# Performance work log

Hardware: AMD Instinct MI355X
Metric: run time of the kernel (lower is better)

## Reference

```python
import jax, jax.numpy as jnp
import numpy as np
import math
from jax import lax

EPS = 1e-5  # BatchNorm1d default eps
K = 7       # causal conv kernel size
H = 5       # number of heads in block 2


def _cconv(x, w, b):
    # CausalConv1d: left-pad by (K-1)*dilation = 6, then valid conv. x: [B,C,L], w: [O,I,K]
    y = lax.conv_general_dilated(x, w, window_strides=(1,), padding=[(K - 1, 0)],
                                 dimension_numbers=('NCH', 'OIH', 'NCH'))
    return y + b[None, :, None]


def _bn(x, g, b):
    # BatchNorm1d in training mode: batch stats over (N, L) per channel, biased variance
    m = x.mean((0, 2), keepdims=True)
    v = ((x - m) ** 2).mean((0, 2), keepdims=True)
    return g[None, :, None] * (x - m) * lax.rsqrt(v + EPS) + b[None, :, None]


def _attn(x1, x2, x3, scale):
    # sigmoid(((X1 @ X2^T) / sqrt(L)) @ X3); x*: [B,C,L]
    s = jnp.einsum('bcl,bdl->bcd', x1, x2) * scale
    return jax.nn.sigmoid(jnp.einsum('bcd,bdl->bcl', s, x3))


def _attn_heads(x1, x2, x3, scale):
    # 5 heads chunked along L (contiguous chunks) -> vectorized over head axis
    B, C, L = x1.shape
    r = lambda x: x.reshape(B, C, H, L // H)
    x1r, x2r, x3r = r(x1), r(x2), r(x3)
    s = jnp.einsum('bchk,bdhk->bhcd', x1r, x2r) * scale  # scale uses full L, as in source
    a = jax.nn.sigmoid(jnp.einsum('bhcd,bdhk->bchk', s, x3r))
    return a.reshape(B, C, L)


def setup_inputs() -> dict:
    key = jax.random.key(0)
    ks = jax.random.split(key, 20)
    B, C, L = 64, 30, 200
    CL = C * L
    cs = (C * K) ** -0.5   # conv weight scale
    ls = CL ** -0.5        # linear weight scale
    d = {}
    d['X'] = jax.random.normal(ks[0], (B, C, L), jnp.float32)
    for i, nm in enumerate(['b1c1', 'b1c2', 'b1c3', 'b2c1', 'b2c2', 'b2c3']):
        d[nm + '_w'] = jax.random.normal(ks[1 + i], (C, C, K), jnp.float32) * cs
        d[nm + '_b'] = jax.random.normal(ks[7 + i], (C,), jnp.float32) * cs
    for nm in ['bn11', 'bn12', 'bn21', 'bn22']:
        d[nm + '_g'] = jnp.ones((C,), jnp.float32)
        d[nm + '_b'] = jnp.zeros((C,), jnp.float32)
    d['lin1_w'] = jax.random.normal(ks[13], (CL, CL), jnp.float32) * ls
    d['lin1_b'] = jax.random.normal(ks[14], (CL,), jnp.float32) * ls
    d['lin2_w'] = jax.random.normal(ks[15], (CL, CL), jnp.float32) * ls
    d['lin2_b'] = jax.random.normal(ks[16], (CL,), jnp.float32) * ls
    d['cw'] = jax.random.normal(ks[17], (CL, 2 * CL), jnp.float32) * (2 * CL) ** -0.5
    d['cb'] = jax.random.normal(ks[18], (CL,), jnp.float32) * (2 * CL) ** -0.5
    return d


def reference(X, b1c1_w, b1c1_b, b1c2_w, b1c2_b, b1c3_w, b1c3_b,
              bn11_g, bn11_b, lin1_w, lin1_b, lin2_w, lin2_b, bn12_g, bn12_b,
              b2c1_w, b2c1_b, b2c2_w, b2c2_b, b2c3_w, b2c3_b,
              bn21_g, bn21_b, bn22_g, bn22_b, cw, cb):
    B, C, L = X.shape
    scale = 1.0 / math.sqrt(L)
    # block 1: single-head sigmoid attention
    a1 = _attn(_cconv(X, b1c1_w, b1c1_b), _cconv(X, b1c2_w, b1c2_b),
               _cconv(X, b1c3_w, b1c3_b), scale)
    a1 = _bn(a1 + X, bn11_g, bn11_b)
    a1f = a1.reshape(B, -1)
    o1 = (a1f @ lin1_w.T + lin1_b) @ lin2_w.T + lin2_b  # dropout is eval-mode identity
    out1 = _bn(a1 + o1.reshape(B, C, L), bn12_g, bn12_b)
    # block 2: 5-head sigmoid attention
    a2 = _attn_heads(_cconv(X, b2c1_w, b2c1_b), _cconv(X, b2c2_w, b2c2_b),
                     _cconv(X, b2c3_w, b2c3_b), scale)
    a2 = _bn(a2 + X, bn21_g, bn21_b)
    a2f = a2.reshape(B, -1)
    # NOTE: source reuses b1_linearchain for block 2 (b2_linearchain is unused)
    o2 = (a2f @ lin1_w.T + lin1_b) @ lin2_w.T + lin2_b
    out2 = _bn(a2 + o2.reshape(B, C, L), bn22_g, bn22_b)
    # converge
    out = jnp.concatenate([out1, out2], axis=1).reshape(B, -1)  # [B, 2*C*L]
    out = out @ cw.T + cb                                       # [B, C*L]
    return out.reshape(B, 30, -1)
```

## Files before the change

### kernel.cpp

```cpp
#include <hip/hip_runtime.h>
#include <hip/hip_bf16.h>
#include <math.h>

typedef __attribute__((ext_vector_type(4))) float f32x4;
typedef __attribute__((ext_vector_type(8))) __bf16 bf16x8;
typedef __attribute__((ext_vector_type(8))) unsigned short u16x8;

__device__ __forceinline__ unsigned short f2bfu(float f) {
    unsigned u = __builtin_bit_cast(unsigned, f);
    u += 0x7fffu + ((u >> 16) & 1u);
    return (unsigned short)(u >> 16);
}

__device__ __forceinline__ bf16x8 to_bf8(f32x4 x, f32x4 y) {
    bf16x8 o;
#pragma unroll
    for (int j = 0; j < 4; ++j) { o[j] = (__bf16)x[j]; o[j + 4] = (__bf16)y[j]; }
    return o;
}

__device__ __forceinline__ void gload_lds16(const void* g, void* l) {
    __builtin_amdgcn_global_load_lds(
        (__attribute__((address_space(1))) const void*)g,
        (__attribute__((address_space(3))) void*)l, 16, 0, 0);
}

template <int N>
__device__ __forceinline__ void waitcnt_vm() {
    if constexpr (N == 6)      asm volatile("s_waitcnt vmcnt(6)" ::: "memory");
    else if constexpr (N == 5) asm volatile("s_waitcnt vmcnt(5)" ::: "memory");
    else                       asm volatile("s_waitcnt vmcnt(0)" ::: "memory");
}

struct ConvArgs {
    const float* w[6];
    const float* b[6];
};

__global__ __launch_bounds__(256) void conv_all(const float* __restrict__ X,
                                                ConvArgs args,
                                                float* __restrict__ out) {
    __shared__ float Xsp[30][208];
    __shared__ float Wg[30][212];
    const int b = blockIdx.x, j = blockIdx.y;
    const int tid = threadIdx.x;
    const float* xb = X + (size_t)b * 6000;
    for (int i = tid; i < 30 * 208; i += 256) {
        const int ci = i / 208, p = i - ci * 208;
        float v = 0.f;
        if (p >= 6 && p < 206) v = xb[ci * 200 + (p - 6)];
        Xsp[ci][p] = v;
    }
    const float* wsrc = args.w[j];
    for (int i = tid; i < 6300; i += 256) Wg[i / 210][i % 210] = wsrc[i];
    __syncthreads();
    if (tid < 240) {
        const int c = tid >> 3;
        const int strip = tid & 7;
        const int l0 = strip * 25;
        float acc[25];
        const float bias = args.b[j][c];
#pragma unroll
        for (int o = 0; o < 25; ++o) acc[o] = bias;
        for (int ci = 0; ci < 30; ++ci) {
            float wv[7];
#pragma unroll
            for (int kk = 0; kk < 7; ++kk) wv[kk] = Wg[c][ci * 7 + kk];
            float xw[31];
#pragma unroll
            for (int i = 0; i < 31; ++i) xw[i] = Xsp[ci][l0 + i];
#pragma unroll
            for (int o = 0; o < 25; ++o) {
                float a = acc[o];
#pragma unroll
                for (int kk = 0; kk < 7; ++kk) a += xw[o + kk] * wv[kk];
                acc[o] = a;
            }
        }
        float* op = out + ((size_t)j * 64 + b) * 6000 + c * 200 + l0;
#pragma unroll
        for (int o = 0; o < 25; ++o) op[o] = acc[o];
    }
}

__global__ __launch_bounds__(256) void attn_k(const float* __restrict__ conv,
                                              const float* __restrict__ X,
                                              float* __restrict__ A_lin) {
    __shared__ float x1s[30][204], x2s[30][204], x3s[30][204];
    __shared__ float S[5][30][30];
    const int b = blockIdx.x, blk = blockIdx.y;
    const int tid = threadIdx.x;
    const f32x4* c1 = (const f32x4*)(conv + (((size_t)blk * 3 + 0) * 64 + b) * 6000);
    const f32x4* c2 = (const f32x4*)(conv + (((size_t)blk * 3 + 1) * 64 + b) * 6000);
    const f32x4* c3 = (const f32x4*)(conv + (((size_t)blk * 3 + 2) * 64 + b) * 6000);
    for (int i = tid; i < 1500; i += 256) {
        const int c = i / 50, q = i - c * 50;
        *(f32x4*)&x1s[c][q * 4] = c1[i];
        *(f32x4*)&x2s[c][q * 4] = c2[i];
        *(f32x4*)&x3s[c][q * 4] = c3[i];
    }
    __syncthreads();
    const float scale = 7.0710678118654752e-2f;
    if (blk == 0) {
        for (int idx = tid; idx < 900; idx += 256) {
            const int c = idx / 30, d = idx - c * 30;
            f32x4 a4 = {};
            for (int q = 0; q < 50; ++q) {
                const f32x4 x = *(const f32x4*)&x1s[c][q * 4];
                const f32x4 y = *(const f32x4*)&x2s[d][q * 4];
                a4 += x * y;
            }
            S[0][c][d] = (a4[0] + a4[1] + a4[2] + a4[3]) * scale;
        }
    } else {
        for (int idx = tid; idx < 4500; idx += 256) {
            const int h = idx / 900, rem = idx - h * 900;
            const int c = rem / 30, d = rem - c * 30;
            f32x4 a4 = {};
            for (int q = 0; q < 10; ++q) {
                const f32x4 x = *(const f32x4*)&x1s[c][h * 40 + q * 4];
                const f32x4 y = *(const f32x4*)&x2s[d][h * 40 + q * 4];
                a4 += x * y;
            }
            S[h][c][d] = (a4[0] + a4[1] + a4[2] + a4[3]) * scale;
        }
    }
    __syncthreads();
    const float* Xb = X + (size_t)b * 6000;
    float* Ab = A_lin + ((size_t)blk * 64 + b) * 6000;
    for (int u = tid; u < 1500; u += 256) {
        const int c = u / 50, q = u - c * 50;
        const int hh = (blk == 0) ? 0 : (q / 10);
        f32x4 a4 = {};
        for (int d = 0; d < 30; ++d) {
            const float sv = S[hh][c][d];
            const f32x4 v = *(const f32x4*)&x3s[d][q * 4];
            a4 += sv * v;
        }
        const f32x4 xv = *(const f32x4*)(Xb + c * 200 + q * 4);
        f32x4 o;
#pragma unroll
        for (int jj = 0; jj < 4; ++jj)
            o[jj] = 1.f / (1.f + __expf(-a4[jj])) + xv[jj];
        *(f32x4*)(Ab + c * 200 + q * 4) = o;
    }
}

template <bool ADD>
__global__ __launch_bounds__(256) void bn_stats(const float* __restrict__ A,
                                                const float* __restrict__ O,
                                                float* __restrict__ part) {
    const int c = blockIdx.x, h = blockIdx.y, bs = blockIdx.z;
    const int tid = threadIdx.x;
    float s = 0.f, ss = 0.f;
    for (int i = tid; i < 1600; i += 256) {
        const int b = bs * 8 + i / 200, l = i % 200;
        const size_t idx = ((size_t)h * 64 + b) * 6000 + c * 200 + l;
        float v = A[idx];
        if constexpr (ADD) v += O[idx];
        s += v; ss += v * v;
    }
    for (int off = 32; off > 0; off >>= 1) { s += __shfl_down(s, off); ss += __shfl_down(ss, off); }
    __shared__ float rs[4], rss[4];
    const int wave = tid >> 6, lane = tid & 63;
    if (lane == 0) { rs[wave] = s; rss[wave] = ss; }
    __syncthreads();
    if (tid == 0) {
        float* p = part + (((size_t)h * 30 + c) * 8 + bs) * 2;
        p[0] = rs[0] + rs[1] + rs[2] + rs[3];
        p[1] = rss[0] + rss[1] + rss[2] + rss[3];
    }
}

__global__ __launch_bounds__(256) void bn_apply1(float* __restrict__ A,
                                                 unsigned short* __restrict__ Ab,
                                                 const float* __restrict__ part,
                                                 const float* __restrict__ g11,
                                                 const float* __restrict__ b11,
                                                 const float* __restrict__ g21,
                                                 const float* __restrict__ b21) {
    const int c = blockIdx.x, h = blockIdx.y, bs = blockIdx.z;
    const int tid = threadIdx.x;
    const float* p = part + (((size_t)h * 30 + c) * 8) * 2;
    float S = 0.f, SS = 0.f;
#pragma unroll
    for (int k = 0; k < 8; ++k) { S += p[k * 2]; SS += p[k * 2 + 1]; }
    const float mean = S * (1.f / 12800.f);
    const float var = SS * (1.f / 12800.f) - mean * mean;
    const float* gp = h ? g21 : g11;
    const float* bp = h ? b21 : b11;
    const float scale = gp[c] * rsqrtf(var + 1e-5f);
    const float shift = bp[c] - mean * scale;
    for (int i = tid; i < 1600; i += 256) {
        const int b = bs * 8 + i / 200, l = i % 200;
        const size_t idx = ((size_t)h * 64 + b) * 6000 + c * 200 + l;
        const float o = A[idx] * scale + shift;
        A[idx] = o;
        Ab[((size_t)h * 64 + b) * 6016 + c * 200 + l] = f2bfu(o);
    }
    if (c == 0) {
        for (int i = tid; i < 8 * 16; i += 256) {
            const int b = bs * 8 + (i >> 4);
            Ab[((size_t)h * 64 + b) * 6016 + 6000 + (i & 15)] = 0;
        }
    }
}

__global__ __launch_bounds__(256) void bn_apply2(const float* __restrict__ A,
                                                 const float* __restrict__ O,
                                                 unsigned short* __restrict__ Cat,
                                                 const float* __restrict__ part,
                                                 const float* __restrict__ g12,
                                                 const float* __restrict__ b12,
                                                 const float* __restrict__ g22,
                                                 const float* __restrict__ b22) {
    const int c = blockIdx.x, h = blockIdx.y, bs = blockIdx.z;
    const int tid = threadIdx.x;
    const float* p = part + (((size_t)h * 30 + c) * 8) * 2;
    float S = 0.f, SS = 0.f;
#pragma unroll
    for (int k = 0; k < 8; ++k) { S += p[k * 2]; SS += p[k * 2 + 1]; }
    const float mean = S * (1.f / 12800.f);
    const float var = SS * (1.f / 12800.f) - mean * mean;
    const float* gp = h ? g22 : g12;
    const float* bp = h ? b22 : b12;
    const float scale = gp[c] * rsqrtf(var + 1e-5f);
    const float shift = bp[c] - mean * scale;
    for (int i = tid; i < 1600; i += 256) {
        const int b = bs * 8 + i / 200, l = i % 200;
        const size_t idx = ((size_t)h * 64 + b) * 6000 + c * 200 + l;
        const float o = (A[idx] + O[idx]) * scale + shift;
        Cat[(size_t)b * 12000 + (size_t)h * 6000 + c * 200 + l] = f2bfu(o);
    }
}

template <int MT>
__global__ __launch_bounds__(256) void gemm_pipe(const unsigned short* __restrict__ A,
                                                 const float* __restrict__ W,
                                                 unsigned short* __restrict__ P,
                                                 int N, int K, int KA,
                                                 int iters_total, int iters_per) {
    constexpr int M = MT * 16;
    constexpr int WB = 128 * 32 * 4;
    constexpr int AB = M * 32 * 2;
    constexpr int ACH = AB / 1024;
    constexpr int BUFSZ = WB + AB;
    constexpr int VMPS = 4 + ACH / 4;
    __shared__ __align__(16) char lds[2][BUFSZ];

    const int tid = threadIdx.x;
    const int wave = tid >> 6;
    const int lane = tid & 63;
    const int r = lane & 15;
    const int g = lane >> 4;
    const int n0 = blockIdx.x * 128;
    const int s = blockIdx.y;
    const int it0 = s * iters_per;
    int it1 = it0 + iters_per;
    if (it1 > iters_total) it1 = iters_total;
    const int nst = it1 - it0;

    f32x4 acc[MT][2] = {};

    const float* wbase[4];
    const float* wclamp[4];
    int kth[4];
#pragma unroll
    for (int u = 0; u < 4; ++u) {
        const int c = wave + 4 * u;
        const int slot = c * 64 + lane;
        const int row = slot >> 3, jj = slot & 7;
        const int j = jj ^ (row & 7);
        int rn = n0 + row;
        if (rn > N - 1) rn = N - 1;
        wbase[u] = W + (size_t)rn * K + j * 4;
        wclamp[u] = W + (size_t)rn * K + (K - 4);
        kth[u] = K - 4 - j * 4;
    }
    const unsigned short* abase[ACH / 4];
#pragma unroll
    for (int u = 0; u < ACH / 4; ++u) {
        const int c = wave + 4 * u;
        const int slot = c * 64 + lane;
        const int m = slot >> 2, jj = slot & 3;
        const int j = jj ^ ((m >> 1) & 3);
        abase[u] = A + (size_t)m * KA + j * 8;
    }

    auto stage = [&](char* base, int it) {
        const int k0 = it * 32;
#pragma unroll
        for (int u = 0; u < 4; ++u) {
            const float* src = (k0 <= kth[u]) ? (wbase[u] + k0) : wclamp[u];
            gload_lds16(src, base + (wave + 4 * u) * 1024);
        }
        char* ab = base + WB;
#pragma unroll
        for (int u = 0; u < ACH / 4; ++u) {
            gload_lds16(abase[u] + k0, ab + (wave + 4 * u) * 1024);
        }
    };

    auto compute = [&](const char* base) {
        const float* Wb = (const float*)base;
        const unsigned short* Ab = (const unsigned short*)(base + WB);
        bf16x8 bfrag[2];
#pragma unroll
        for (int nt = 0; nt < 2; ++nt) {
            const int wr = (wave + 4 * nt) * 16 + r;
            const f32x4* Wrow = (const f32x4*)(Wb + wr * 32);
            bfrag[nt] = to_bf8(Wrow[(2 * g) ^ (r & 7)], Wrow[(2 * g + 1) ^ (r & 7)]);
        }
#pragma unroll
        for (int mt = 0; mt < MT; ++mt) {
            const int m = mt * 16 + r;
            const bf16x8 afrag = __builtin_bit_cast(
                bf16x8, ((const u16x8*)(Ab + (size_t)m * 32))[g ^ ((m >> 1) & 3)]);
            acc[mt][0] = __builtin_amdgcn_mfma_f32_16x16x32_bf16(afrag, bfrag[0], acc[mt][0], 0, 0, 0);
            acc[mt][1] = __builtin_amdgcn_mfma_f32_16x16x32_bf16(afrag, bfrag[1], acc[mt][1], 0, 0, 0);
        }
    };

    if (nst > 0) {
        stage(&lds[0][0], it0);
        if (nst > 1) {
            stage(&lds[1][0], it0 + 1);
            waitcnt_vm<VMPS>();
        } else {
            waitcnt_vm<0>();
        }
        __builtin_amdgcn_s_barrier();
        __builtin_amdgcn_sched_barrier(0);

        int cur = 0;
        for (int it = it0; it < it1; ++it) {
            compute(&lds[cur][0]);
            __builtin_amdgcn_sched_barrier(0);
            __builtin_amdgcn_s_barrier();
            if (it + 2 < it1) stage(&lds[cur][0], it + 2);
            if (it + 1 < it1) {
                if (it + 2 < it1) waitcnt_vm<VMPS>();
                else              waitcnt_vm<0>();
                __builtin_amdgcn_s_barrier();
                __builtin_amdgcn_sched_barrier(0);
            }
            cur ^= 1;
        }
    }

    unsigned short* Pp = P + (size_t)s * M * N;
#pragma unroll
    for (int nt = 0; nt < 2; ++nt) {
        const int col = n0 + (wave + 4 * nt) * 16 + r;
        if (col < N) {
#pragma unroll
            for (int mt = 0; mt < MT; ++mt) {
#pragma unroll
                for (int rr = 0; rr < 4; ++rr) {
                    const int row = mt * 16 + g * 4 + rr;
                    Pp[(size_t)row * N + col] = f2bfu(acc[mt][nt][rr]);
                }
            }
        }
    }
}

template <bool OUT_BF16>
__global__ __launch_bounds__(256) void reduce_bias(const unsigned short* __restrict__ P,
                                                   const float* __restrict__ bias,
                                                   int KS, int MN, int N, int KOUT,
                                                   float* __restrict__ of,
                                                   unsigned short* __restrict__ ob) {
    const int gid0 = blockIdx.x * 256 + threadIdx.x;
    const int gstr = gridDim.x * 256;
    for (int idx = gid0; idx < MN; idx += gstr) {
        float v = bias[idx % N];
        for (int s = 0; s < KS; ++s) {
            const unsigned u = P[(size_t)s * MN + idx];
            v += __builtin_bit_cast(float, u << 16);
        }
        if constexpr (OUT_BF16) ob[(size_t)(idx / N) * KOUT + (idx % N)] = f2bfu(v);
        else of[idx] = v;
    }
    if constexpr (OUT_BF16) {
        if (KOUT > N) {
            const int M = MN / N, PADW = KOUT - N;
            for (int i = gid0; i < M * PADW; i += gstr)
                ob[(size_t)(i / PADW) * KOUT + N + (i % PADW)] = 0;
        }
    }
}

extern "C" void kernel_launch(void* const* d_in, const int* in_sizes, int n_in,
                              void* d_out, int out_size, void* d_ws, size_t ws_size,
                              hipStream_t stream) {
    (void)in_sizes; (void)n_in; (void)out_size;
    const float* X = (const float*)d_in[0];
    ConvArgs ca;
    for (int j = 0; j < 6; ++j) {
        ca.w[j] = (const float*)d_in[1 + 2 * j];
        ca.b[j] = (const float*)d_in[2 + 2 * j];
    }
    const float* bn11_g = (const float*)d_in[13];
    const float* bn11_b = (const float*)d_in[14];
    const float* bn12_g = (const float*)d_in[15];
    const float* bn12_b = (const float*)d_in[16];
    const float* bn21_g = (const float*)d_in[17];
    const float* bn21_b = (const float*)d_in[18];
    const float* bn22_g = (const float*)d_in[19];
    const float* bn22_b = (const float*)d_in[20];
    const float* lin1_w = (const float*)d_in[21];
    const float* lin1_b = (const float*)d_in[22];
    const float* lin2_w = (const float*)d_in[23];
    const float* lin2_b = (const float*)d_in[24];
    const float* cw = (const float*)d_in[25];
    const float* cb = (const float*)d_in[26];
    float* out = (float*)d_out;

    char* w = (char*)d_ws;
    float* A_lin = (float*)w;
    unsigned short* A_bf = (unsigned short*)(w + 3072000);
    char* U = w + 4612096;
    float* convout = (float*)U;
    unsigned short* T_bf = (unsigned short*)U;
    float* O = (float*)(U + 1540096);
    unsigned short* Cat = (unsigned short*)(U + 4612096);
    float* BNS = (float*)(w + 13828096);
    unsigned short* P = (unsigned short*)(w + 13832192);

    const size_t avail = ws_size > 13832192 ? ws_size - 13832192 : 0;
    int KS12 = (int)(avail / 1536000);
    if (KS12 > 16) KS12 = 16;
    if (KS12 < 1) KS12 = 1;
    int KS3 = (int)(avail / 768000);
    if (KS3 > 20) KS3 = 20;
    if (KS3 < 1) KS3 = 1;

    conv_all<<<dim3(64, 6), 256, 0, stream>>>(X, ca, convout);
    attn_k<<<dim3(64, 2), 256, 0, stream>>>(convout, X, A_lin);
    bn_stats<false><<<dim3(30, 2, 8), 256, 0, stream>>>(A_lin, nullptr, BNS);
    bn_apply1<<<dim3(30, 2, 8), 256, 0, stream>>>(A_lin, A_bf, BNS, bn11_g, bn11_b, bn21_g, bn21_b);

    {
        const int it_tot = 188;
        const int it_per = (it_tot + KS12 - 1) / KS12;
        gemm_pipe<8><<<dim3(47, KS12), 256, 0, stream>>>(A_bf, lin1_w, P, 6000, 6000, 6016, it_tot, it_per);
        reduce_bias<true><<<dim3(768), 256, 0, stream>>>(P, lin1_b, KS12, 768000, 6000, 6016, nullptr, T_bf);
        gemm_pipe<8><<<dim3(47, KS12), 256, 0, stream>>>(T_bf, lin2_w, P, 6000, 6000, 6016, it_tot, it_per);
        reduce_bias<false><<<dim3(768), 256, 0, stream>>>(P, lin2_b, KS12, 768000, 6000, 6000, O, nullptr);
    }

    bn_stats<true><<<dim3(30, 2, 8), 256, 0, stream>>>(A_lin, O, BNS);
    bn_apply2<<<dim3(30, 2, 8), 256, 0, stream>>>(A_lin, O, Cat, BNS, bn12_g, bn12_b, bn22_g, bn22_b);

    {
        const int it_tot = 375;
        const int it_per = (it_tot + KS3 - 1) / KS3;
        gemm_pipe<4><<<dim3(47, KS3), 256, 0, stream>>>(Cat, cw, P, 6000, 12000, 12000, it_tot, it_per);
        reduce_bias<false><<<dim3(768), 256, 0, stream>>>(P, cb, KS3, 384000, 6000, 6000, out, nullptr);
    }
}
```

Measured before the change: 262.0 us.

## Triple-buffer GEMM pipeline, fuse BN stats into apply, lower split-K

The GEMM LDS pipeline grows from double to triple buffering, with prefetch depth 3 and vmcnt waits that depend on how many newer stages are in flight. The separate BN statistics kernels are removed: each apply block now recomputes the full per-channel statistics redundantly, which saves two launches at the cost of about eight times more reads. The split-K factors are capped at 10 instead of 16 and 20, which cuts partial-sum traffic for the reduce kernels but lowers parallelism. The larger LDS footprint may reduce occupancy.

```diff
diff --git a/kernel.cpp b/kernel.cpp
--- a/kernel.cpp
+++ b/kernel.cpp
@@ -25,11 +25,17 @@
         (__attribute__((address_space(3))) void*)l, 16, 0, 0);
 }
 
-template <int N>
-__device__ __forceinline__ void waitcnt_vm() {
-    if constexpr (N == 6)      asm volatile("s_waitcnt vmcnt(6)" ::: "memory");
-    else if constexpr (N == 5) asm volatile("s_waitcnt vmcnt(5)" ::: "memory");
-    else                       asm volatile("s_waitcnt vmcnt(0)" ::: "memory");
+template <int VMPS>
+__device__ __forceinline__ void wait_newer(int newer) {
+    if (newer >= 2) {
+        if constexpr (VMPS == 6) asm volatile("s_waitcnt vmcnt(12)" ::: "memory");
+        else                     asm volatile("s_waitcnt vmcnt(10)" ::: "memory");
+    } else if (newer == 1) {
+        if constexpr (VMPS == 6) asm volatile("s_waitcnt vmcnt(6)" ::: "memory");
+        else                     asm volatile("s_waitcnt vmcnt(5)" ::: "memory");
+    } else {
+        asm volatile("s_waitcnt vmcnt(0)" ::: "memory");
+    }
 }
 
 struct ConvArgs {
@@ -146,51 +152,40 @@
     }
 }
 
-template <bool ADD>
-__global__ __launch_bounds__(256) void bn_stats(const float* __restrict__ A,
-                                                const float* __restrict__ O,
-                                                float* __restrict__ part) {
-    const int c = blockIdx.x, h = blockIdx.y, bs = blockIdx.z;
-    const int tid = threadIdx.x;
-    float s = 0.f, ss = 0.f;
-    for (int i = tid; i < 1600; i += 256) {
-        const int b = bs * 8 + i / 200, l = i % 200;
-        const size_t idx = ((size_t)h * 64 + b) * 6000 + c * 200 + l;
-        float v = A[idx];
-        if constexpr (ADD) v += O[idx];
-        s += v; ss += v * v;
-    }
-    for (int off = 32; off > 0; off >>= 1) { s += __shfl_down(s, off); ss += __shfl_down(ss, off); }
-    __shared__ float rs[4], rss[4];
-    const int wave = tid >> 6, lane = tid & 63;
-    if (lane == 0) { rs[wave] = s; rss[wave] = ss; }
-    __syncthreads();
-    if (tid == 0) {
-        float* p = part + (((size_t)h * 30 + c) * 8 + bs) * 2;
-        p[0] = rs[0] + rs[1] + rs[2] + rs[3];
-        p[1] = rss[0] + rss[1] + rss[2] + rss[3];
-    }
-}
-
-__global__ __launch_bounds__(256) void bn_apply1(float* __restrict__ A,
+__global__ __launch_bounds__(256) void bn_fused1(float* __restrict__ A,
                                                  unsigned short* __restrict__ Ab,
-                                                 const float* __restrict__ part,
                                                  const float* __restrict__ g11,
                                                  const float* __restrict__ b11,
                                                  const float* __restrict__ g21,
                                                  const float* __restrict__ b21) {
     const int c = blockIdx.x, h = blockIdx.y, bs = blockIdx.z;
     const int tid = threadIdx.x;
-    const float* p = part + (((size_t)h * 30 + c) * 8) * 2;
-    float S = 0.f, SS = 0.f;
-#pragma unroll
-    for (int k = 0; k < 8; ++k) { S += p[k * 2]; SS += p[k * 2 + 1]; }
-    const float mean = S * (1.f / 12800.f);
-    const float var = SS * (1.f / 12800.f) - mean * mean;
-    const float* gp = h ? g21 : g11;
-    const float* bp = h ? b21 : b11;
-    const float scale = gp[c] * rsqrtf(var + 1e-5f);
-    const float shift = bp[c] - mean * scale;
+    const size_t cbase = (size_t)h * 64 * 6000 + c * 200;
+    float s = 0.f, ss = 0.f;
+    for (int i = tid; i < 12800; i += 256) {
+        const int b = i / 200, l = i - b * 200;
+        const float v = A[cbase + (size_t)b * 6000 + l];
+        s += v; ss += v * v;
+    }
+    for (int off = 32; off > 0; off >>= 1) { s += __shfl_down(s, off); ss += __shfl_down(ss, off); }
+    __shared__ float rs[4], rss[4];
+    __shared__ float sc_sh, sh_sh;
+    const int wave = tid >> 6, lane = tid & 63;
+    if (lane == 0) { rs[wave] = s; rss[wave] = ss; }
+    __syncthreads();
+    if (tid == 0) {
+        const float S = rs[0] + rs[1] + rs[2] + rs[3];
+        const float SS = rss[0] + rss[1] + rss[2] + rss[3];
+        const float mean = S * (1.f / 12800.f);
+        const float var = SS * (1.f / 12800.f) - mean * mean;
+        const float* gp = h ? g21 : g11;
+        const float* bp = h ? b21 : b11;
+        const float scale = gp[c] * rsqrtf(var + 1e-5f);
+        sc_sh = scale;
+        sh_sh = bp[c] - mean * scale;
+    }
+    __syncthreads();
+    const float scale = sc_sh, shift = sh_sh;
     for (int i = tid; i < 1600; i += 256) {
         const int b = bs * 8 + i / 200, l = i % 200;
         const size_t idx = ((size_t)h * 64 + b) * 6000 + c * 200 + l;
@@ -206,26 +201,42 @@
     }
 }
 
-__global__ __launch_bounds__(256) void bn_apply2(const float* __restrict__ A,
+__global__ __launch_bounds__(256) void bn_fused2(const float* __restrict__ A,
                                                  const float* __restrict__ O,
                                                  unsigned short* __restrict__ Cat,
-                                                 const float* __restrict__ part,
                                                  const float* __restrict__ g12,
                                                  const float* __restrict__ b12,
                                                  const float* __restrict__ g22,
                                                  const float* __restrict__ b22) {
     const int c = blockIdx.x, h = blockIdx.y, bs = blockIdx.z;
     const int tid = threadIdx.x;
-    const float* p = part + (((size_t)h * 30 + c) * 8) * 2;
-    float S = 0.f, SS = 0.f;
-#pragma unroll
-    for (int k = 0; k < 8; ++k) { S += p[k * 2]; SS += p[k * 2 + 1]; }
-    const float mean = S * (1.f / 12800.f);
-    const float var = SS * (1.f / 12800.f) - mean * mean;
-    const float* gp = h ? g22 : g12;
-    const float* bp = h ? b22 : b12;
-    const float scale = gp[c] * rsqrtf(var + 1e-5f);
-    const float shift = bp[c] - mean * scale;
+    const size_t cbase = (size_t)h * 64 * 6000 + c * 200;
+    float s = 0.f, ss = 0.f;
+    for (int i = tid; i < 12800; i += 256) {
+        const int b = i / 200, l = i - b * 200;
+        const size_t idx = cbase + (size_t)b * 6000 + l;
+        const float v = A[idx] + O[idx];
+        s += v; ss += v * v;
+    }
+    for (int off = 32; off > 0; off >>= 1) { s += __shfl_down(s, off); ss += __shfl_down(ss, off); }
+    __shared__ float rs[4], rss[4];
+    __shared__ float sc_sh, sh_sh;
+    const int wave = tid >> 6, lane = tid & 63;
+    if (lane == 0) { rs[wave] = s; rss[wave] = ss; }
+    __syncthreads();
+    if (tid == 0) {
+        const float S = rs[0] + rs[1] + rs[2] + rs[3];
+        const float SS = rss[0] + rss[1] + rss[2] + rss[3];
+        const float mean = S * (1.f / 12800.f);
+        const float var = SS * (1.f / 12800.f) - mean * mean;
+        const float* gp = h ? g22 : g12;
+        const float* bp = h ? b22 : b12;
+        const float scale = gp[c] * rsqrtf(var + 1e-5f);
+        sc_sh = scale;
+        sh_sh = bp[c] - mean * scale;
+    }
+    __syncthreads();
+    const float scale = sc_sh, shift = sh_sh;
     for (int i = tid; i < 1600; i += 256) {
         const int b = bs * 8 + i / 200, l = i % 200;
         const size_t idx = ((size_t)h * 64 + b) * 6000 + c * 200 + l;
@@ -246,7 +257,7 @@
     constexpr int ACH = AB / 1024;
     constexpr int BUFSZ = WB + AB;
     constexpr int VMPS = 4 + ACH / 4;
-    __shared__ __align__(16) char lds[2][BUFSZ];
+    __shared__ __align__(16) char lds[3][BUFSZ];
 
     const int tid = threadIdx.x;
     const int wave = tid >> 6;
@@ -322,29 +333,28 @@
     };
 
     if (nst > 0) {
+        const int p = nst < 3 ? nst : 3;
         stage(&lds[0][0], it0);
-        if (nst > 1) {
-            stage(&lds[1][0], it0 + 1);
-            waitcnt_vm<VMPS>();
-        } else {
-            waitcnt_vm<0>();
-        }
+        if (p > 1) stage(&lds[1][0], it0 + 1);
+        if (p > 2) stage(&lds[2][0], it0 + 2);
+        wait_newer<VMPS>(p - 1);
         __builtin_amdgcn_s_barrier();
         __builtin_amdgcn_sched_barrier(0);
 
-        int cur = 0;
+        int bi = 0;
         for (int it = it0; it < it1; ++it) {
-            compute(&lds[cur][0]);
+            compute(&lds[bi][0]);
             __builtin_amdgcn_sched_barrier(0);
             __builtin_amdgcn_s_barrier();
-            if (it + 2 < it1) stage(&lds[cur][0], it + 2);
+            if (it + 3 < it1) stage(&lds[bi][0], it + 3);
             if (it + 1 < it1) {
-                if (it + 2 < it1) waitcnt_vm<VMPS>();
-                else              waitcnt_vm<0>();
+                const int last = it1 - 1;
+                const int newer = ((it + 3 < last ? it + 3 : last)) - (it + 1);
+                wait_newer<VMPS>(newer);
                 __builtin_amdgcn_s_barrier();
                 __builtin_amdgcn_sched_barrier(0);
             }
-            cur ^= 1;
+            bi = bi == 2 ? 0 : bi + 1;
         }
     }
 
@@ -425,21 +435,19 @@
     unsigned short* T_bf = (unsigned short*)U;
     float* O = (float*)(U + 1540096);
     unsigned short* Cat = (unsigned short*)(U + 4612096);
-    float* BNS = (float*)(w + 13828096);
     unsigned short* P = (unsigned short*)(w + 13832192);
 
     const size_t avail = ws_size > 13832192 ? ws_size - 13832192 : 0;
     int KS12 = (int)(avail / 1536000);
-    if (KS12 > 16) KS12 = 16;
+    if (KS12 > 10) KS12 = 10;
     if (KS12 < 1) KS12 = 1;
     int KS3 = (int)(avail / 768000);
-    if (KS3 > 20) KS3 = 20;
+    if (KS3 > 10) KS3 = 10;
     if (KS3 < 1) KS3 = 1;
 
     conv_all<<<dim3(64, 6), 256, 0, stream>>>(X, ca, convout);
     attn_k<<<dim3(64, 2), 256, 0, stream>>>(convout, X, A_lin);
-    bn_stats<false><<<dim3(30, 2, 8), 256, 0, stream>>>(A_lin, nullptr, BNS);
-    bn_apply1<<<dim3(30, 2, 8), 256, 0, stream>>>(A_lin, A_bf, BNS, bn11_g, bn11_b, bn21_g, bn21_b);
+    bn_fused1<<<dim3(30, 2, 8), 256, 0, stream>>>(A_lin, A_bf, bn11_g, bn11_b, bn21_g, bn21_b);
 
     {
         const int it_tot = 188;
@@ -450,8 +458,7 @@
         reduce_bias<false><<<dim3(768), 256, 0, stream>>>(P, lin2_b, KS12, 768000, 6000, 6000, O, nullptr);
     }
 
-    bn_stats<true><<<dim3(30, 2, 8), 256, 0, stream>>>(A_lin, O, BNS);
-    bn_apply2<<<dim3(30, 2, 8), 256, 0, stream>>>(A_lin, O, Cat, BNS, bn12_g, bn12_b, bn22_g, bn22_b);
+    bn_fused2<<<dim3(30, 2, 8), 256, 0, stream>>>(A_lin, O, Cat, bn12_g, bn12_b, bn22_g, bn22_b);
 
     {
         const int it_tot = 375;
```

Result: no change. 257.9 us (-1.6%).
